# Performance work log

Hardware: AMD Instinct MI355X
Metric: run time of the kernel (lower is better)

The kernel has to match this reference:

```python
import jax, jax.numpy as jnp
import numpy as np

STEP = 20
SCORING_WEIGHT = 0.01


def quaternion_matrix(q):
    # q: [..., 4] normalized quaternion; replicates the module's exact formula.
    q0, q1, q2, q3 = q[..., 0], q[..., 1], q[..., 2], q[..., 3]
    R = jnp.stack([
        1.0 - 2.0 * (q2 ** 2 + q3 ** 2),
        2.0 * q1 * q2 - 2.0 * q0 * q3,
        2.0 * q0 * q2 + 2.0 * q1 * q3,
        2.0 * q1 * q2 + 2.0 * q3 * q0,
        1.0 - 2.0 * (q1 ** 2 + q3 ** 2),
        -2.0 * q0 * q1 + 2.0 * q2 * q3,
        -2.0 * q0 * q2 + 2.0 * q1 * q3,
        2.0 * q0 * q1 + 2.0 * q2 * q3,
        1.0 - 2.0 * (q1 ** 2 + q2 ** 2),
    ], axis=-1)
    return R.reshape(R.shape[:-1] + (3, 3))


def setup_inputs() -> dict:
    key = jax.random.key(0)
    ks = jax.random.split(key, 8)
    bs, h, w, P = 8, 32, 32, 512
    pred_r = jax.random.normal(ks[0], (bs, 4, h, w), dtype=jnp.float32)
    pred_t = jax.random.normal(ks[1], (bs, 3, h, w), dtype=jnp.float32)
    pred_s = jax.random.uniform(ks[2], (bs, 1, h, w), dtype=jnp.float32, minval=0.05, maxval=1.0)
    mask = jnp.ones((bs, 1, h, w), dtype=jnp.float32)
    gt_r = jax.random.normal(ks[3], (bs, 3, 3), dtype=jnp.float32)
    gt_t = jax.random.normal(ks[4], (bs, 3), dtype=jnp.float32)
    model_xyz = jax.random.normal(ks[5], (bs, 3, P), dtype=jnp.float32)
    cls_ids = jnp.zeros((bs,), dtype=jnp.int64 if jax.config.jax_enable_x64 else jnp.int32)
    return {"pred_r": pred_r, "pred_t": pred_t, "pred_s": pred_s, "mask": mask,
            "gt_r": gt_r, "gt_t": gt_t, "model_xyz": model_xyz, "cls_ids": cls_ids}


def reference(pred_r, pred_t, pred_s, mask, gt_r, gt_t, model_xyz, cls_ids):
    bs, _, h, w = pred_r.shape
    hw = h * w
    # normalize quaternion per pixel
    q = pred_r / jnp.linalg.norm(pred_r, axis=1, keepdims=True)
    q = q.reshape(bs, 4, hw)
    t = pred_t.reshape(bs, 3, hw)
    s = pred_s.reshape(bs, hw)
    # all-ones mask -> valid pixels are arange(hw); stride-step subsample (as in torch code)
    idx = np.arange(hw // STEP) * STEP  # N = 51 static indices
    pr = q[:, :, idx]                   # [bs,4,N]
    pt = t[:, :, idx]                   # [bs,3,N]
    ps = s[:, idx]                      # [bs,N]
    R_pre = quaternion_matrix(jnp.transpose(pr, (0, 2, 1)))  # [bs,N,3,3]
    # transform model points
    pred = jnp.einsum('bnij,bjp->bnip', R_pre, model_xyz) \
        + jnp.transpose(pt, (0, 2, 1))[:, :, :, None]         # [bs,N,3,P]
    gt = jnp.einsum('bij,bjp->bip', gt_r, model_xyz) + gt_t[:, :, None]  # [bs,3,P]
    # ADD-S: min over gt points of pairwise distance (Chamfer one-sided)
    pn = jnp.sum(pred ** 2, axis=2)                 # [bs,N,P]
    gn = jnp.sum(gt ** 2, axis=1)                   # [bs,P]
    cross = jnp.einsum('bnip,biq->bnpq', pred, gt)  # [bs,N,P,P]
    d2 = pn[..., None] + gn[:, None, None, :] - 2.0 * cross
    dmin = jnp.sqrt(jnp.maximum(jnp.min(d2, axis=-1), 0.0))  # [bs,N,P]
    add_ij = jnp.mean(dmin, axis=-1)                # [bs,N]
    sub_loss = jnp.mean(add_ij * ps - SCORING_WEIGHT * jnp.log(ps), axis=1)  # [bs]
    gadd_loss = jnp.mean(sub_loss)
    gadd_loss = jnp.where(jnp.isinf(gadd_loss), 0.0, gadd_loss)
    gadd_loss = jnp.where(jnp.isnan(gadd_loss), 0.0, gadd_loss)
    return gadd_loss
```

## Files before the change

kernel.cpp:

```cpp
#include <hip/hip_runtime.h>
#include <math.h>

#define BS   8
#define HW   1024
#define NP   512
#define NS   51
#define STEP 20
#define SW   0.01f

__global__ __launch_bounds__(256) void add_loss_kernel(
    const float* __restrict__ pred_r,
    const float* __restrict__ pred_t,
    const float* __restrict__ pred_s,
    const float* __restrict__ gt_r,
    const float* __restrict__ gt_t,
    const float* __restrict__ model_xyz,
    float* __restrict__ partials)
{
    const int bn  = blockIdx.x;
    const int b   = bn / NS;
    const int n   = bn % NS;
    const int pix = n * STEP;
    const int tid = threadIdx.x;

    __shared__ float gx[NP], gy[NP], gz[NP];

    const float* Rg = gt_r + b * 9;
    const float g00 = Rg[0], g01 = Rg[1], g02 = Rg[2];
    const float g10 = Rg[3], g11 = Rg[4], g12 = Rg[5];
    const float g20 = Rg[6], g21 = Rg[7], g22 = Rg[8];
    const float tx = gt_t[b*3+0], ty = gt_t[b*3+1], tz = gt_t[b*3+2];
    const float* M = model_xyz + b * 3 * NP;

    for (int p = tid; p < NP; p += 256) {
        const float mx = M[p], my = M[NP + p], mz = M[2*NP + p];
        gx[p] = fmaf(g00, mx, fmaf(g01, my, fmaf(g02, mz, tx)));
        gy[p] = fmaf(g10, mx, fmaf(g11, my, fmaf(g12, mz, ty)));
        gz[p] = fmaf(g20, mx, fmaf(g21, my, fmaf(g22, mz, tz)));
    }

    float q0 = pred_r[(b*4 + 0)*HW + pix];
    float q1 = pred_r[(b*4 + 1)*HW + pix];
    float q2 = pred_r[(b*4 + 2)*HW + pix];
    float q3 = pred_r[(b*4 + 3)*HW + pix];
    const float inv = rsqrtf(q0*q0 + q1*q1 + q2*q2 + q3*q3);
    q0 *= inv; q1 *= inv; q2 *= inv; q3 *= inv;
    const float r00 = 1.f - 2.f*(q2*q2 + q3*q3);
    const float r01 = 2.f*q1*q2 - 2.f*q0*q3;
    const float r02 = 2.f*q0*q2 + 2.f*q1*q3;
    const float r10 = 2.f*q1*q2 + 2.f*q3*q0;
    const float r11 = 1.f - 2.f*(q1*q1 + q3*q3);
    const float r12 = -2.f*q0*q1 + 2.f*q2*q3;
    const float r20 = -2.f*q0*q2 + 2.f*q1*q3;
    const float r21 = 2.f*q0*q1 + 2.f*q2*q3;
    const float r22 = 1.f - 2.f*(q1*q1 + q2*q2);
    const float ptx = pred_t[(b*3 + 0)*HW + pix];
    const float pty = pred_t[(b*3 + 1)*HW + pix];
    const float ptz = pred_t[(b*3 + 2)*HW + pix];

    const int p0 = tid, p1 = tid + 256;
    float mx0 = M[p0], my0 = M[NP + p0], mz0 = M[2*NP + p0];
    float mx1 = M[p1], my1 = M[NP + p1], mz1 = M[2*NP + p1];
    const float px0 = fmaf(r00, mx0, fmaf(r01, my0, fmaf(r02, mz0, ptx)));
    const float py0 = fmaf(r10, mx0, fmaf(r11, my0, fmaf(r12, mz0, pty)));
    const float pz0 = fmaf(r20, mx0, fmaf(r21, my0, fmaf(r22, mz0, ptz)));
    const float px1 = fmaf(r00, mx1, fmaf(r01, my1, fmaf(r02, mz1, ptx)));
    const float py1 = fmaf(r10, mx1, fmaf(r11, my1, fmaf(r12, mz1, pty)));
    const float pz1 = fmaf(r20, mx1, fmaf(r21, my1, fmaf(r22, mz1, ptz)));

    __syncthreads();

    float dmin0 = 3.4e38f, dmin1 = 3.4e38f;
    #pragma unroll 4
    for (int j = 0; j < NP; ++j) {
        const float gxj = gx[j], gyj = gy[j], gzj = gz[j];
        float dx = px0 - gxj, dy = py0 - gyj, dz = pz0 - gzj;
        float d2 = fmaf(dx, dx, fmaf(dy, dy, dz*dz));
        dmin0 = fminf(dmin0, d2);
        dx = px1 - gxj; dy = py1 - gyj; dz = pz1 - gzj;
        d2 = fmaf(dx, dx, fmaf(dy, dy, dz*dz));
        dmin1 = fminf(dmin1, d2);
    }

    float sum = sqrtf(fmaxf(dmin0, 0.f)) + sqrtf(fmaxf(dmin1, 0.f));

    for (int off = 32; off; off >>= 1) sum += __shfl_down(sum, off, 64);
    __shared__ float wsum[4];
    if ((tid & 63) == 0) wsum[tid >> 6] = sum;
    __syncthreads();
    if (tid == 0) {
        const float s = wsum[0] + wsum[1] + wsum[2] + wsum[3];
        const float add_ij = s * (1.f / NP);
        const float ps = pred_s[b * HW + pix];
        partials[bn] = add_ij * ps - SW * logf(ps);
    }
}

__global__ __launch_bounds__(512) void finalize_kernel(
    const float* __restrict__ partials, float* __restrict__ out)
{
    const int tid = threadIdx.x;
    float v = (tid < BS * NS) ? partials[tid] : 0.f;
    for (int off = 32; off; off >>= 1) v += __shfl_down(v, off, 64);
    __shared__ float ws[8];
    if ((tid & 63) == 0) ws[tid >> 6] = v;
    __syncthreads();
    if (tid == 0) {
        float s = 0.f;
        #pragma unroll
        for (int i = 0; i < 8; ++i) s += ws[i];
        s *= 1.f / (float)(BS * NS);
        if (isinf(s) || isnan(s)) s = 0.f;
        out[0] = s;
    }
}

extern "C" void kernel_launch(void* const* d_in, const int* in_sizes, int n_in,
                              void* d_out, int out_size, void* d_ws, size_t ws_size,
                              hipStream_t stream) {
    const float* pred_r    = (const float*)d_in[0];
    const float* pred_t    = (const float*)d_in[1];
    const float* pred_s    = (const float*)d_in[2];
    const float* gt_r      = (const float*)d_in[4];
    const float* gt_t      = (const float*)d_in[5];
    const float* model_xyz = (const float*)d_in[6];

    float* partials = (float*)d_ws;
    float* out      = (float*)d_out;

    add_loss_kernel<<<BS * NS, 256, 0, stream>>>(
        pred_r, pred_t, pred_s, gt_r, gt_t, model_xyz, partials);
    finalize_kernel<<<1, 512, 0, stream>>>(partials, out);
}
```

Before: 88.89 us.

## Precompute GT points in prep kernel, stream via float4 global loads, fuse finalize with atomics

The ground-truth transform moves into a small prep kernel that writes the transformed points to workspace. The scan kernel then reads them with wavefront-uniform float4 global loads instead of staging them in shared memory, and keeps four independent min accumulators per point. The finalize kernel is replaced by an atomic sum plus a last-block-done counter. The aim is to remove the per-block redundant GT transform, the shared-memory sync and one launch, at the cost of an extra small prep launch, global/cache loads inside the inner loop, and an atomic summation order that is not deterministic.

```diff
diff --git a/kernel.cpp b/kernel.cpp
--- a/kernel.cpp
+++ b/kernel.cpp
@@ -7,37 +7,53 @@
 #define NS   51
 #define STEP 20
 #define SW   0.01f
+#define HDR  16
+#define BSTRIDE (3*NP)
 
-__global__ __launch_bounds__(256) void add_loss_kernel(
+__global__ __launch_bounds__(128) void prep_kernel(
+    const float* __restrict__ gt_r,
+    const float* __restrict__ gt_t,
+    const float* __restrict__ model_xyz,
+    float* __restrict__ ws)
+{
+    const int b = blockIdx.x;
+    const int tid = threadIdx.x;
+    if (b == 0 && tid == 0) {
+        ws[0] = 0.0f;
+        ((unsigned int*)ws)[1] = 0u;
+    }
+    const float* Rg = gt_r + b * 9;
+    const float g00 = Rg[0], g01 = Rg[1], g02 = Rg[2];
+    const float g10 = Rg[3], g11 = Rg[4], g12 = Rg[5];
+    const float g20 = Rg[6], g21 = Rg[7], g22 = Rg[8];
+    const float tx = gt_t[b*3+0], ty = gt_t[b*3+1], tz = gt_t[b*3+2];
+    const float* M = model_xyz + b * 3 * NP;
+    float* gx = ws + HDR + b * BSTRIDE;
+    float* gy = gx + NP;
+    float* gz = gx + 2 * NP;
+    #pragma unroll
+    for (int p = tid; p < NP; p += 128) {
+        const float mx = M[p], my = M[NP + p], mz = M[2*NP + p];
+        gx[p] = fmaf(g00, mx, fmaf(g01, my, fmaf(g02, mz, tx)));
+        gy[p] = fmaf(g10, mx, fmaf(g11, my, fmaf(g12, mz, ty)));
+        gz[p] = fmaf(g20, mx, fmaf(g21, my, fmaf(g22, mz, tz)));
+    }
+}
+
+__global__ __launch_bounds__(256) void scan_kernel(
     const float* __restrict__ pred_r,
     const float* __restrict__ pred_t,
     const float* __restrict__ pred_s,
-    const float* __restrict__ gt_r,
-    const float* __restrict__ gt_t,
     const float* __restrict__ model_xyz,
-    float* __restrict__ partials)
+    const float* __restrict__ ws_ro,
+    float* __restrict__ ws,
+    float* __restrict__ out)
 {
     const int bn  = blockIdx.x;
     const int b   = bn / NS;
     const int n   = bn % NS;
     const int pix = n * STEP;
     const int tid = threadIdx.x;
-
-    __shared__ float gx[NP], gy[NP], gz[NP];
-
-    const float* Rg = gt_r + b * 9;
-    const float g00 = Rg[0], g01 = Rg[1], g02 = Rg[2];
-    const float g10 = Rg[3], g11 = Rg[4], g12 = Rg[5];
-    const float g20 = Rg[6], g21 = Rg[7], g22 = Rg[8];
-    const float tx = gt_t[b*3+0], ty = gt_t[b*3+1], tz = gt_t[b*3+2];
-    const float* M = model_xyz + b * 3 * NP;
-
-    for (int p = tid; p < NP; p += 256) {
-        const float mx = M[p], my = M[NP + p], mz = M[2*NP + p];
-        gx[p] = fmaf(g00, mx, fmaf(g01, my, fmaf(g02, mz, tx)));
-        gy[p] = fmaf(g10, mx, fmaf(g11, my, fmaf(g12, mz, ty)));
-        gz[p] = fmaf(g20, mx, fmaf(g21, my, fmaf(g22, mz, tz)));
-    }
 
     float q0 = pred_r[(b*4 + 0)*HW + pix];
     float q1 = pred_r[(b*4 + 1)*HW + pix];
@@ -58,9 +74,10 @@
     const float pty = pred_t[(b*3 + 1)*HW + pix];
     const float ptz = pred_t[(b*3 + 2)*HW + pix];
 
+    const float* M = model_xyz + b * 3 * NP;
     const int p0 = tid, p1 = tid + 256;
-    float mx0 = M[p0], my0 = M[NP + p0], mz0 = M[2*NP + p0];
-    float mx1 = M[p1], my1 = M[NP + p1], mz1 = M[2*NP + p1];
+    const float mx0 = M[p0], my0 = M[NP + p0], mz0 = M[2*NP + p0];
+    const float mx1 = M[p1], my1 = M[NP + p1], mz1 = M[2*NP + p1];
     const float px0 = fmaf(r00, mx0, fmaf(r01, my0, fmaf(r02, mz0, ptx)));
     const float py0 = fmaf(r10, mx0, fmaf(r11, my0, fmaf(r12, mz0, pty)));
     const float pz0 = fmaf(r20, mx0, fmaf(r21, my0, fmaf(r22, mz0, ptz)));
@@ -68,19 +85,39 @@
     const float py1 = fmaf(r10, mx1, fmaf(r11, my1, fmaf(r12, mz1, pty)));
     const float pz1 = fmaf(r20, mx1, fmaf(r21, my1, fmaf(r22, mz1, ptz)));
 
-    __syncthreads();
+    const float4* __restrict__ gx4 = (const float4*)(ws_ro + HDR + b * BSTRIDE);
+    const float4* __restrict__ gy4 = gx4 + NP/4;
+    const float4* __restrict__ gz4 = gy4 + NP/4;
 
-    float dmin0 = 3.4e38f, dmin1 = 3.4e38f;
+    const float BIG = 3.4e38f;
+    float4 m0 = make_float4(BIG, BIG, BIG, BIG);
+    float4 m1 = make_float4(BIG, BIG, BIG, BIG);
+
     #pragma unroll 4
-    for (int j = 0; j < NP; ++j) {
-        const float gxj = gx[j], gyj = gy[j], gzj = gz[j];
-        float dx = px0 - gxj, dy = py0 - gyj, dz = pz0 - gzj;
-        float d2 = fmaf(dx, dx, fmaf(dy, dy, dz*dz));
-        dmin0 = fminf(dmin0, d2);
-        dx = px1 - gxj; dy = py1 - gyj; dz = pz1 - gzj;
-        d2 = fmaf(dx, dx, fmaf(dy, dy, dz*dz));
-        dmin1 = fminf(dmin1, d2);
+    for (int j = 0; j < NP/4; ++j) {
+        const float4 X = gx4[j];
+        const float4 Y = gy4[j];
+        const float4 Z = gz4[j];
+        float dx, dy, dz, d2;
+        dx = px0 - X.x; dy = py0 - Y.x; dz = pz0 - Z.x;
+        d2 = fmaf(dx, dx, fmaf(dy, dy, dz*dz)); m0.x = fminf(m0.x, d2);
+        dx = px0 - X.y; dy = py0 - Y.y; dz = pz0 - Z.y;
+        d2 = fmaf(dx, dx, fmaf(dy, dy, dz*dz)); m0.y = fminf(m0.y, d2);
+        dx = px0 - X.z; dy = py0 - Y.z; dz = pz0 - Z.z;
+        d2 = fmaf(dx, dx, fmaf(dy, dy, dz*dz)); m0.z = fminf(m0.z, d2);
+        dx = px0 - X.w; dy = py0 - Y.w; dz = pz0 - Z.w;
+        d2 = fmaf(dx, dx, fmaf(dy, dy, dz*dz)); m0.w = fminf(m0.w, d2);
+        dx = px1 - X.x; dy = py1 - Y.x; dz = pz1 - Z.x;
+        d2 = fmaf(dx, dx, fmaf(dy, dy, dz*dz)); m1.x = fminf(m1.x, d2);
+        dx = px1 - X.y; dy = py1 - Y.y; dz = pz1 - Z.y;
+        d2 = fmaf(dx, dx, fmaf(dy, dy, dz*dz)); m1.y = fminf(m1.y, d2);
+        dx = px1 - X.z; dy = py1 - Y.z; dz = pz1 - Z.z;
+        d2 = fmaf(dx, dx, fmaf(dy, dy, dz*dz)); m1.z = fminf(m1.z, d2);
+        dx = px1 - X.w; dy = py1 - Y.w; dz = pz1 - Z.w;
+        d2 = fmaf(dx, dx, fmaf(dy, dy, dz*dz)); m1.w = fminf(m1.w, d2);
     }
+    const float dmin0 = fminf(fminf(m0.x, m0.y), fminf(m0.z, m0.w));
+    const float dmin1 = fminf(fminf(m1.x, m1.y), fminf(m1.z, m1.w));
 
     float sum = sqrtf(fmaxf(dmin0, 0.f)) + sqrtf(fmaxf(dmin1, 0.f));
 
@@ -92,26 +129,16 @@
         const float s = wsum[0] + wsum[1] + wsum[2] + wsum[3];
         const float add_ij = s * (1.f / NP);
         const float ps = pred_s[b * HW + pix];
-        partials[bn] = add_ij * ps - SW * logf(ps);
-    }
-}
-
-__global__ __launch_bounds__(512) void finalize_kernel(
-    const float* __restrict__ partials, float* __restrict__ out)
-{
-    const int tid = threadIdx.x;
-    float v = (tid < BS * NS) ? partials[tid] : 0.f;
-    for (int off = 32; off; off >>= 1) v += __shfl_down(v, off, 64);
-    __shared__ float ws[8];
-    if ((tid & 63) == 0) ws[tid >> 6] = v;
-    __syncthreads();
-    if (tid == 0) {
-        float s = 0.f;
-        #pragma unroll
-        for (int i = 0; i < 8; ++i) s += ws[i];
-        s *= 1.f / (float)(BS * NS);
-        if (isinf(s) || isnan(s)) s = 0.f;
-        out[0] = s;
+        const float term = add_ij * ps - SW * logf(ps);
+        atomicAdd(ws, term);
+        __threadfence();
+        const unsigned int old = atomicAdd(((unsigned int*)ws) + 1, 1u);
+        if (old == (unsigned int)(BS * NS - 1)) {
+            float total = atomicAdd(ws, 0.0f);
+            total *= 1.f / (float)(BS * NS);
+            if (isinf(total) || isnan(total)) total = 0.f;
+            out[0] = total;
+        }
     }
 }
 
@@ -125,10 +152,10 @@
     const float* gt_t      = (const float*)d_in[5];
     const float* model_xyz = (const float*)d_in[6];
 
-    float* partials = (float*)d_ws;
-    float* out      = (float*)d_out;
+    float* ws  = (float*)d_ws;
+    float* out = (float*)d_out;
 
-    add_loss_kernel<<<BS * NS, 256, 0, stream>>>(
-        pred_r, pred_t, pred_s, gt_r, gt_t, model_xyz, partials);
-    finalize_kernel<<<1, 512, 0, stream>>>(partials, out);
+    prep_kernel<<<BS, 128, 0, stream>>>(gt_r, gt_t, model_xyz, ws);
+    scan_kernel<<<BS * NS, 256, 0, stream>>>(
+        pred_r, pred_t, pred_s, model_xyz, ws, ws, out);
 }
```

After: 99.84 us. +12.3%, slower.
